# Performance work log

Measured on AMD Instinct MI355X. Metric: run time of the kernel, lower is better.

The kernel has to match this reference:

```python
import jax, jax.numpy as jnp
import numpy as np


def setup_inputs() -> dict:
    key = jax.random.key(0)
    k1, k2 = jax.random.split(key)
    B, D = 8192, 256
    pred = jax.random.normal(k1, (B, D), dtype=jnp.float32)
    gt = jax.random.normal(k2, (B, D), dtype=jnp.float32)
    sigma = jnp.ones((), dtype=jnp.float32)  # learned scalar param (dim=1, mode='auto')
    return {"pred": pred, "gt": gt, "sigma": sigma}


def reference(pred, gt, sigma):
    # p, g: [B, D] (flatten from start_dim=1 is identity for 2D inputs)
    p = pred.reshape(pred.shape[0], -1)
    g = gt.reshape(gt.shape[0], -1)
    B, D = p.shape
    noise_var = sigma ** 2
    # MVN(mean=p_i, cov=noise_var*I).log_prob(g_j) in closed form:
    # -0.5 * ||g_j - p_i||^2 / noise_var - 0.5 * D * log(2*pi*noise_var)
    sq_dist = (
        jnp.sum(p * p, axis=-1)[:, None]
        + jnp.sum(g * g, axis=-1)[None, :]
        - 2.0 * (p @ g.T)
    )  # [B, B]
    log_norm = 0.5 * D * jnp.log(2.0 * jnp.pi * noise_var)
    logits = -0.5 * sq_dist / noise_var - log_norm  # [B, B], class dim = 1
    # cross_entropy(logits, arange(B)) = mean_i(-log_softmax(logits)[i, i])
    logp = jax.nn.log_softmax(logits, axis=1)
    loss = -jnp.mean(jnp.diagonal(logp))
    loss = loss * jax.lax.stop_gradient(2.0 * noise_var)
    return loss
```

## Files before the change

### kernel.cpp

```cpp
#include <hip/hip_runtime.h>
#include <hip/hip_fp8.h>


typedef float f32x4 __attribute__((ext_vector_type(4)));
typedef float f32x16 __attribute__((ext_vector_type(16)));
typedef long llong2 __attribute__((ext_vector_type(2)));

#define LN2F 0.6931471805599453f
#define LOG2EF 1.4426950408889634f
#define NB 8192
#define ND 256
#define NCHUNK 32

#define AS1 __attribute__((address_space(1)))
#define AS3 __attribute__((address_space(3)))

__device__ __forceinline__ float fexp2(float x) {
#if __has_builtin(__builtin_amdgcn_exp2f)
  return __builtin_amdgcn_exp2f(x);
#else
  float r;
  asm("v_exp_f32 %0, %1\n\ts_nop 1" : "=v"(r) : "v"(x));
  return r;
#endif
}

__device__ __forceinline__ int pack4_fp8(float a, float b, float c, float d) {
#if __has_builtin(__builtin_amdgcn_cvt_pk_fp8_f32)
  int w = __builtin_amdgcn_cvt_pk_fp8_f32(a, b, 0, false);
  w = __builtin_amdgcn_cvt_pk_fp8_f32(c, d, w, true);
  return w;
#else
  unsigned b0 = __hip_fp8_e4m3(a).__x, b1 = __hip_fp8_e4m3(b).__x;
  unsigned b2 = __hip_fp8_e4m3(c).__x, b3 = __hip_fp8_e4m3(d).__x;
  return (int)(b0 | (b1 << 8) | (b2 << 16) | (b3 << 24));
#endif
}

__global__ __launch_bounds__(256) void vmse_prep(
    const float* __restrict__ pred, const float* __restrict__ gt,
    const float* __restrict__ sigma,
    unsigned char* __restrict__ Ah, unsigned char* __restrict__ Bh,
    float* __restrict__ diag, float* __restrict__ gnorm,
    float* __restrict__ ghs)
{
  const float nv = sigma[0] * sigma[0];
  const float s = LOG2EF / nv;
  const int row = blockIdx.x * 4 + (threadIdx.x >> 6);
  const int l = threadIdx.x & 63;
  const float4 p = *(const float4*)(pred + row * ND + l * 4);
  const float4 g = *(const float4*)(gt   + row * ND + l * 4);
  const int pw = pack4_fp8(p.x * s, p.y * s, p.z * s, p.w * s);
  const int gw = pack4_fp8(g.x, g.y, g.z, g.w);
  const int pos = (l >> 3) * 32 + ((l >> 1) & 1) * 16 + ((l >> 2) & 1) * 8 + (l & 1) * 4;
  *(int*)(Ah + row * ND + pos) = pw;
  *(int*)(Bh + row * ND + pos) = gw;
  float dd = p.x * g.x + p.y * g.y + p.z * g.z + p.w * g.w;
  float gg = g.x * g.x + g.y * g.y + g.z * g.z + g.w * g.w;
  #pragma unroll
  for (int off = 1; off < 64; off <<= 1) {
    dd += __shfl_xor(dd, off);
    gg += __shfl_xor(gg, off);
  }
  if (l == 0) {
    diag[row] = dd;
    gnorm[row] = gg;
    ghs[row] = -0.5f * s * gg;
  }
}

__global__ __launch_bounds__(512, 4) void vmse_main(
    const unsigned char* __restrict__ Ah, const unsigned char* __restrict__ Bh,
    const float* __restrict__ ghs, float* __restrict__ partial)
{
  __shared__ unsigned char lds[8][32 * 256];
  __shared__ float lds_ghs[256];
  const int tid = threadIdx.x;
  const int lane = tid & 63;
  const int wid = tid >> 6;
  const int rb = blockIdx.x & 31;
  const int ch = blockIdx.x >> 5;
  const int r31 = lane & 31;
  const int hi = lane >> 5;
  const int j0 = ch * 256;

  {
    const int r = wid * 4 + (lane >> 4);
    const int cg = (lane & 15) ^ (r & 7);
    const unsigned char* src = Bh + (size_t)(j0 + r) * ND + cg * 16;
    #pragma unroll
    for (int t = 0; t < 8; ++t)
      __builtin_amdgcn_global_load_lds(
          (const AS1 unsigned int*)(src + t * 8192),
          (AS3 unsigned int*)&lds[t][wid * 1024], 16, 0, 0);
  }
  if (tid < 256) lds_ghs[tid] = ghs[j0 + tid];

  long pf[16];
  {
    const unsigned char* prow = Ah + (size_t)((rb * 256) + (wid * 32) + r31) * ND;
    #pragma unroll
    for (int t2 = 0; t2 < 8; ++t2) {
      const llong2 v = *(const llong2*)(prow + t2 * 32 + hi * 16);
      pf[2 * t2] = v[0];
      pf[2 * t2 + 1] = v[1];
    }
  }

  const int r0b = r31 & 1;
  const int q2 = (r31 >> 1) & 3;
  const char* base = (const char*)&lds[0][0] + r31 * 256 + (hi ^ r0b) * 16;
  const char* pq[4];
  #pragma unroll
  for (int b = 0; b < 4; ++b) pq[b] = base + ((b ^ q2) * 32);

  float m2 = -3.0e38f, l2 = 0.0f;

  __syncthreads();

  const char* gbase = (const char*)lds_ghs + hi * 16;
  #pragma unroll
  for (int tile = 0; tile < 8; ++tile) {
    f32x16 acc;
    #pragma unroll
    for (int q = 0; q < 4; ++q) {
      const f32x4 gv = *(const f32x4*)(gbase + tile * 128 + q * 32);
      acc[4 * q + 0] = gv[0];
      acc[4 * q + 1] = gv[1];
      acc[4 * q + 2] = gv[2];
      acc[4 * q + 3] = gv[3];
    }
    __builtin_amdgcn_s_setprio(1);
    #pragma unroll
    for (int a = 0; a < 2; ++a) {
      #pragma unroll
      for (int b = 0; b < 4; ++b) {
        const llong2 g = *(const llong2*)(pq[b] + a * 128 + tile * 8192);
        const int t = 2 * (a * 4 + b);
        acc = __builtin_amdgcn_mfma_f32_32x32x16_fp8_fp8(g[0], pf[t], acc, 0, 0, 0);
        acc = __builtin_amdgcn_mfma_f32_32x32x16_fp8_fp8(g[1], pf[t + 1], acc, 0, 0, 0);
      }
    }
    __builtin_amdgcn_s_setprio(0);
    float mx0 = fmaxf(fmaxf(acc[0], acc[1]), fmaxf(acc[2], acc[3]));
    float mx1 = fmaxf(fmaxf(acc[4], acc[5]), fmaxf(acc[6], acc[7]));
    float mx2 = fmaxf(fmaxf(acc[8], acc[9]), fmaxf(acc[10], acc[11]));
    float mx3 = fmaxf(fmaxf(acc[12], acc[13]), fmaxf(acc[14], acc[15]));
    const float tmax = fmaxf(fmaxf(mx0, mx1), fmaxf(mx2, mx3));
    if (__any(tmax > m2 + 8.0f)) {
      const float nm = fmaxf(m2, tmax);
      l2 *= fexp2(m2 - nm);
      m2 = nm;
    }
    float e0 = (fexp2(acc[0] - m2) + fexp2(acc[1] - m2)) +
               (fexp2(acc[2] - m2) + fexp2(acc[3] - m2));
    float e1 = (fexp2(acc[4] - m2) + fexp2(acc[5] - m2)) +
               (fexp2(acc[6] - m2) + fexp2(acc[7] - m2));
    float e2 = (fexp2(acc[8] - m2) + fexp2(acc[9] - m2)) +
               (fexp2(acc[10] - m2) + fexp2(acc[11] - m2));
    float e3 = (fexp2(acc[12] - m2) + fexp2(acc[13] - m2)) +
               (fexp2(acc[14] - m2) + fexp2(acc[15] - m2));
    l2 += (e0 + e1) + (e2 + e3);
  }

  {
    const float om = __shfl_xor(m2, 32);
    const float ol = __shfl_xor(l2, 32);
    const float nm = fmaxf(m2, om);
    l2 = l2 * fexp2(m2 - nm) + ol * fexp2(om - nm);
    m2 = nm;
    if (hi == 0) {
      const int row = rb * 256 + wid * 32 + r31;
      partial[row * NCHUNK + ch] = m2 + log2f(l2);
    }
  }
}

__global__ __launch_bounds__(256) void vmse_combine(
    const float* __restrict__ partial, const float* __restrict__ diag,
    const float* __restrict__ gnorm, const float* __restrict__ sigma,
    float* __restrict__ bsum)
{
  const int r = blockIdx.x * 256 + threadIdx.x;
  const float nv = sigma[0] * sigma[0];
  float p[NCHUNK];
  float M = -3.0e38f;
  #pragma unroll
  for (int c = 0; c < NCHUNK; ++c) { p[c] = partial[r * NCHUNK + c]; M = fmaxf(M, p[c]); }
  float ssum = 0.f;
  #pragma unroll
  for (int c = 0; c < NCHUNK; ++c) ssum += exp2f(p[c] - M);
  const float lse2 = M + log2f(ssum);
  const float zii = (diag[r] - 0.5f * gnorm[r]) / nv;
  float contrib = LN2F * lse2 - zii;
  #pragma unroll
  for (int off = 1; off < 64; off <<= 1) contrib += __shfl_xor(contrib, off);
  __shared__ float wsum[4];
  if ((threadIdx.x & 63) == 0) wsum[threadIdx.x >> 6] = contrib;
  __syncthreads();
  if (threadIdx.x == 0)
    bsum[blockIdx.x] = (wsum[0] + wsum[1]) + (wsum[2] + wsum[3]);
}

__global__ __launch_bounds__(64) void vmse_final(
    const float* __restrict__ bsum, const float* __restrict__ sigma,
    float* __restrict__ out)
{
  const int lane = threadIdx.x;
  float v = (lane < 32) ? bsum[lane] : 0.f;
  #pragma unroll
  for (int off = 1; off < 64; off <<= 1) v += __shfl_xor(v, off);
  if (lane == 0) {
    const float nv = sigma[0] * sigma[0];
    out[0] = v * (2.0f * nv / (float)NB);
  }
}

extern "C" void kernel_launch(void* const* d_in, const int* in_sizes, int n_in,
                              void* d_out, int out_size, void* d_ws, size_t ws_size,
                              hipStream_t stream)
{
  const float* pred  = (const float*)d_in[0];
  const float* gt    = (const float*)d_in[1];
  const float* sigma = (const float*)d_in[2];
  char* ws = (char*)d_ws;
  unsigned char* Ah = (unsigned char*)(ws);
  unsigned char* Bh = (unsigned char*)(ws + (2u << 20));
  float* gnorm   = (float*)(ws + (4u << 20));
  float* diag    = (float*)(ws + (4u << 20) + (32u << 10));
  float* ghs     = (float*)(ws + (4u << 20) + (64u << 10));
  float* partial = (float*)(ws + (4u << 20) + (96u << 10));
  float* bsum    = (float*)(ws + (4u << 20) + (96u << 10) + (1u << 20));

  vmse_prep<<<NB / 4, 256, 0, stream>>>(pred, gt, sigma, Ah, Bh, diag, gnorm, ghs);
  vmse_main<<<32 * NCHUNK, 512, 0, stream>>>(Ah, Bh, ghs, partial);
  vmse_combine<<<NB / 256, 256, 0, stream>>>(partial, diag, gnorm, sigma, bsum);
  vmse_final<<<1, 64, 0, stream>>>(bsum, sigma, (float*)d_out);
}
```

Baseline: 44.38 us.

## Double per-wave row tile so each LDS B fragment feeds two MFMA chains

Each wave now computes 64 rows (two 32-row sub-tiles) instead of 32, so every B fragment read from LDS is reused for two independent MFMA accumulators. This halves the grid to 512 blocks and halves LDS staging traffic per output element, and the two interleaved accumulator chains hide MFMA latency better. In exchange it roughly doubles register pressure for the A fragments and accumulators, and there are fewer blocks to fill the CUs.

Measured after the change: 53.08 us. 19.6% more time.

```diff
diff --git a/kernel.cpp b/kernel.cpp
--- a/kernel.cpp
+++ b/kernel.cpp
@@ -69,6 +69,28 @@
   }
 }
 
+__device__ __forceinline__ void epi16(const f32x16& acc, float& m, float& l) {
+  const float mx0 = fmaxf(fmaxf(acc[0], acc[1]), fmaxf(acc[2], acc[3]));
+  const float mx1 = fmaxf(fmaxf(acc[4], acc[5]), fmaxf(acc[6], acc[7]));
+  const float mx2 = fmaxf(fmaxf(acc[8], acc[9]), fmaxf(acc[10], acc[11]));
+  const float mx3 = fmaxf(fmaxf(acc[12], acc[13]), fmaxf(acc[14], acc[15]));
+  const float tmax = fmaxf(fmaxf(mx0, mx1), fmaxf(mx2, mx3));
+  if (__any(tmax > m + 8.0f)) {
+    const float nm = fmaxf(m, tmax);
+    l *= fexp2(m - nm);
+    m = nm;
+  }
+  const float e0 = (fexp2(acc[0] - m) + fexp2(acc[1] - m)) +
+                   (fexp2(acc[2] - m) + fexp2(acc[3] - m));
+  const float e1 = (fexp2(acc[4] - m) + fexp2(acc[5] - m)) +
+                   (fexp2(acc[6] - m) + fexp2(acc[7] - m));
+  const float e2 = (fexp2(acc[8] - m) + fexp2(acc[9] - m)) +
+                   (fexp2(acc[10] - m) + fexp2(acc[11] - m));
+  const float e3 = (fexp2(acc[12] - m) + fexp2(acc[13] - m)) +
+                   (fexp2(acc[14] - m) + fexp2(acc[15] - m));
+  l += (e0 + e1) + (e2 + e3);
+}
+
 __global__ __launch_bounds__(512, 4) void vmse_main(
     const unsigned char* __restrict__ Ah, const unsigned char* __restrict__ Bh,
     const float* __restrict__ ghs, float* __restrict__ partial)
@@ -78,8 +100,8 @@
   const int tid = threadIdx.x;
   const int lane = tid & 63;
   const int wid = tid >> 6;
-  const int rb = blockIdx.x & 31;
-  const int ch = blockIdx.x >> 5;
+  const int rb = blockIdx.x & 15;
+  const int ch = blockIdx.x >> 4;
   const int r31 = lane & 31;
   const int hi = lane >> 5;
   const int j0 = ch * 256;
@@ -96,14 +118,16 @@
   }
   if (tid < 256) lds_ghs[tid] = ghs[j0 + tid];
 
-  long pf[16];
-  {
-    const unsigned char* prow = Ah + (size_t)((rb * 256) + (wid * 32) + r31) * ND;
+  long pf[2][16];
+  #pragma unroll
+  for (int s = 0; s < 2; ++s) {
+    const unsigned char* prow =
+        Ah + (size_t)((rb * 512) + (wid * 64) + (s * 32) + r31) * ND;
     #pragma unroll
     for (int t2 = 0; t2 < 8; ++t2) {
       const llong2 v = *(const llong2*)(prow + t2 * 32 + hi * 16);
-      pf[2 * t2] = v[0];
-      pf[2 * t2 + 1] = v[1];
+      pf[s][2 * t2] = v[0];
+      pf[s][2 * t2 + 1] = v[1];
     }
   }
 
@@ -114,22 +138,24 @@
   #pragma unroll
   for (int b = 0; b < 4; ++b) pq[b] = base + ((b ^ q2) * 32);
 
-  float m2 = -3.0e38f, l2 = 0.0f;
+  float m2[2] = {-3.0e38f, -3.0e38f};
+  float l2[2] = {0.0f, 0.0f};
 
   __syncthreads();
 
   const char* gbase = (const char*)lds_ghs + hi * 16;
   #pragma unroll
   for (int tile = 0; tile < 8; ++tile) {
-    f32x16 acc;
+    f32x16 acc0, acc1;
     #pragma unroll
     for (int q = 0; q < 4; ++q) {
       const f32x4 gv = *(const f32x4*)(gbase + tile * 128 + q * 32);
-      acc[4 * q + 0] = gv[0];
-      acc[4 * q + 1] = gv[1];
-      acc[4 * q + 2] = gv[2];
-      acc[4 * q + 3] = gv[3];
-    }
+      acc0[4 * q + 0] = gv[0];
+      acc0[4 * q + 1] = gv[1];
+      acc0[4 * q + 2] = gv[2];
+      acc0[4 * q + 3] = gv[3];
+    }
+    acc1 = acc0;
     __builtin_amdgcn_s_setprio(1);
     #pragma unroll
     for (int a = 0; a < 2; ++a) {
@@ -137,41 +163,28 @@
       for (int b = 0; b < 4; ++b) {
         const llong2 g = *(const llong2*)(pq[b] + a * 128 + tile * 8192);
         const int t = 2 * (a * 4 + b);
-        acc = __builtin_amdgcn_mfma_f32_32x32x16_fp8_fp8(g[0], pf[t], acc, 0, 0, 0);
-        acc = __builtin_amdgcn_mfma_f32_32x32x16_fp8_fp8(g[1], pf[t + 1], acc, 0, 0, 0);
+        acc0 = __builtin_amdgcn_mfma_f32_32x32x16_fp8_fp8(g[0], pf[0][t], acc0, 0, 0, 0);
+        acc1 = __builtin_amdgcn_mfma_f32_32x32x16_fp8_fp8(g[0], pf[1][t], acc1, 0, 0, 0);
+        acc0 = __builtin_amdgcn_mfma_f32_32x32x16_fp8_fp8(g[1], pf[0][t + 1], acc0, 0, 0, 0);
+        acc1 = __builtin_amdgcn_mfma_f32_32x32x16_fp8_fp8(g[1], pf[1][t + 1], acc1, 0, 0, 0);
       }
     }
     __builtin_amdgcn_s_setprio(0);
-    float mx0 = fmaxf(fmaxf(acc[0], acc[1]), fmaxf(acc[2], acc[3]));
-    float mx1 = fmaxf(fmaxf(acc[4], acc[5]), fmaxf(acc[6], acc[7]));
-    float mx2 = fmaxf(fmaxf(acc[8], acc[9]), fmaxf(acc[10], acc[11]));
-    float mx3 = fmaxf(fmaxf(acc[12], acc[13]), fmaxf(acc[14], acc[15]));
-    const float tmax = fmaxf(fmaxf(mx0, mx1), fmaxf(mx2, mx3));
-    if (__any(tmax > m2 + 8.0f)) {
-      const float nm = fmaxf(m2, tmax);
-      l2 *= fexp2(m2 - nm);
-      m2 = nm;
-    }
-    float e0 = (fexp2(acc[0] - m2) + fexp2(acc[1] - m2)) +
-               (fexp2(acc[2] - m2) + fexp2(acc[3] - m2));
-    float e1 = (fexp2(acc[4] - m2) + fexp2(acc[5] - m2)) +
-               (fexp2(acc[6] - m2) + fexp2(acc[7] - m2));
-    float e2 = (fexp2(acc[8] - m2) + fexp2(acc[9] - m2)) +
-               (fexp2(acc[10] - m2) + fexp2(acc[11] - m2));
-    float e3 = (fexp2(acc[12] - m2) + fexp2(acc[13] - m2)) +
-               (fexp2(acc[14] - m2) + fexp2(acc[15] - m2));
-    l2 += (e0 + e1) + (e2 + e3);
-  }
-
-  {
-    const float om = __shfl_xor(m2, 32);
-    const float ol = __shfl_xor(l2, 32);
-    const float nm = fmaxf(m2, om);
-    l2 = l2 * fexp2(m2 - nm) + ol * fexp2(om - nm);
-    m2 = nm;
+    epi16(acc0, m2[0], l2[0]);
+    epi16(acc1, m2[1], l2[1]);
+  }
+
+  #pragma unroll
+  for (int s = 0; s < 2; ++s) {
+    float m = m2[s], l = l2[s];
+    const float om = __shfl_xor(m, 32);
+    const float ol = __shfl_xor(l, 32);
+    const float nm = fmaxf(m, om);
+    l = l * fexp2(m - nm) + ol * fexp2(om - nm);
+    m = nm;
     if (hi == 0) {
-      const int row = rb * 256 + wid * 32 + r31;
-      partial[row * NCHUNK + ch] = m2 + log2f(l2);
+      const int row = rb * 512 + wid * 64 + s * 32 + r31;
+      partial[row * NCHUNK + ch] = m + log2f(l);
     }
   }
 }
@@ -233,7 +246,7 @@
   float* bsum    = (float*)(ws + (4u << 20) + (96u << 10) + (1u << 20));
 
   vmse_prep<<<NB / 4, 256, 0, stream>>>(pred, gt, sigma, Ah, Bh, diag, gnorm, ghs);
-  vmse_main<<<32 * NCHUNK, 512, 0, stream>>>(Ah, Bh, ghs, partial);
+  vmse_main<<<16 * NCHUNK, 512, 0, stream>>>(Ah, Bh, ghs, partial);
   vmse_combine<<<NB / 256, 256, 0, stream>>>(partial, diag, gnorm, sigma, bsum);
   vmse_final<<<1, 64, 0, stream>>>(bsum, sigma, (float*)d_out);
 }
```
